# Kernel optimization log

Measured on AMD Instinct MI355X. Metric: run time of the kernel, lower is better.

Reference implementation:

```python
import jax, jax.numpy as jnp
import numpy as np

B, S, NH, NKV, D = 2, 2048, 32, 8, 128

def setup_inputs() -> dict:
    key = jax.random.key(0)
    kq, kk, kv = jax.random.split(key, 3)
    query = jax.random.normal(kq, (B, S, NH, D), dtype=jnp.float32)
    k_ = jax.random.normal(kk, (B, S, NKV, D), dtype=jnp.float32)
    v_ = jax.random.normal(kv, (B, S, NKV, D), dtype=jnp.float32)
    # causal additive mask, broadcastable to [B, NH, S, S]
    causal = jnp.tril(jnp.ones((S, S), dtype=bool))
    attn_mask = jnp.where(causal, 0.0, -1e9).astype(jnp.float32)[None, None]
    return {"query": query, "key": k_, "value": v_, "attn_mask": attn_mask}

def reference(query, key, value, attn_mask):
    nh, nkv = query.shape[-2], key.shape[-2]
    # [B, S, H, D] -> [B, H, S, D]
    q = jnp.swapaxes(query, -3, -2)
    k = jnp.swapaxes(key, -3, -2)
    v = jnpp_swap(value) if False else jnp.swapaxes(value, -3, -2)
    qpk = nh // nkv
    if qpk > 1:
        k = jnp.repeat(k, qpk, axis=-3)
        v = jnp.repeat(v, qpk, axis=-3)
    scale = q.shape[-1] ** (-0.5)
    # [B, H, Sq, Sk]
    score = jnp.einsum('bhqd,bhkd->bhqk', q, k) * scale
    score = score + attn_mask
    probs = jax.nn.softmax(score.astype(jnp.float32), axis=-1).astype(q.dtype)
    out = jnp.einsum('bhqk,bhkd->bhqd', probs, v)
    # [B, H, S, D] -> [B, S, H, D]
    return jnp.swapaxes(out, 1, 2)
```

## Files before the change

### kernel.cpp

```cpp
#include <hip/hip_runtime.h>
#include <hip/hip_bf16.h>

#define B_    2
#define S_    2048
#define NH_   32
#define NKV_  8
#define D_    128
#define QBLK  128
#define KVBLK 64

#define KVH_STRIDE 524288u
#define V_WS_OFF   8388608u

typedef __bf16 bf16x8 __attribute__((ext_vector_type(8)));
typedef float  f32x16 __attribute__((ext_vector_type(16)));
typedef unsigned short u16x4 __attribute__((ext_vector_type(4)));
typedef unsigned int   u32x4 __attribute__((ext_vector_type(4)));

typedef const __attribute__((address_space(1))) void* gptr_t;
typedef __attribute__((address_space(3))) void*       lptr_t;

#if __has_builtin(__builtin_amdgcn_exp2f)
#define EXP2(x) __builtin_amdgcn_exp2f(x)
#else
#define EXP2(x) exp2f(x)
#endif

__device__ inline unsigned short bfu(float f) {
    return __builtin_bit_cast(unsigned short, (__bf16)f);
}
__device__ inline unsigned packbf(float lo, float hi) {
    return (unsigned)bfu(lo) | ((unsigned)bfu(hi) << 16);
}

__global__ __launch_bounds__(256)
void convert_kv(const float* __restrict__ kin, const float* __restrict__ vin,
                unsigned short* __restrict__ kout, unsigned short* __restrict__ vout) {
    __shared__ unsigned short vl[64][136];
    const int t = threadIdx.x;
    if (blockIdx.x < 4096) {
        const int g = blockIdx.x * 256 + t;
        const size_t o = (size_t)g * 4;
        const int d   = (int)(o & 127);
        const int k   = (int)((o >> 7) & 2047);
        const int kvh = (int)((o >> 18) & 7);
        const int b   = (int)(o >> 21);
        const float* src = kin + (((size_t)(b * 2048 + k)) * 8 + kvh) * 128 + d;
        float4 x = *reinterpret_cast<const float4*>(src);
        u16x4 u = { bfu(x.x), bfu(x.y), bfu(x.z), bfu(x.w) };
        *reinterpret_cast<u16x4*>(kout + o) = u;
        return;
    }
    const int bb = blockIdx.x - 4096;
    const int j  = bb & 31;
    const int bk = bb >> 5;
    const int b  = bk >> 3, kvh = bk & 7;
    const float* base = vin + (((size_t)(b * 2048 + j * 64)) * 8 + kvh) * 128;
    #pragma unroll
    for (int i = 0; i < 8; ++i) {
        const int row = i * 8 + (t >> 5), c4 = t & 31;
        float4 x = *reinterpret_cast<const float4*>(base + (size_t)row * 1024 + c4 * 4);
        u16x4 u = { bfu(x.x), bfu(x.y), bfu(x.z), bfu(x.w) };
        *reinterpret_cast<u16x4*>(&vl[row][c4 * 4]) = u;
    }
    __syncthreads();
    unsigned short* out = vout + (size_t)bb * 8192;
    #pragma unroll
    for (int it = 0; it < 4; ++it) {
        const int c = it * 256 + t;
        const int d = c >> 3, k0 = (c & 7) * 8;
        u16x4 lo = { vl[k0 + 0][d], vl[k0 + 1][d], vl[k0 + 2][d], vl[k0 + 3][d] };
        u16x4 hi = { vl[k0 + 4][d], vl[k0 + 5][d], vl[k0 + 6][d], vl[k0 + 7][d] };
        *reinterpret_cast<u16x4*>(out + (size_t)d * 64 + k0)     = lo;
        *reinterpret_cast<u16x4*>(out + (size_t)d * 64 + k0 + 4) = hi;
    }
}

__global__ __launch_bounds__(256, 2)
void sdpa_fwd(const float* __restrict__ qg, const unsigned short* __restrict__ kws,
              const unsigned short* __restrict__ vws, float* __restrict__ og)
{
    __shared__ __align__(16) unsigned short Kb[2][8192];
    __shared__ __align__(16) unsigned short Vb[2][8192];

    const int bx  = blockIdx.x;
    const int qt  = 15 - (bx >> 6);
    const int r   = bx & 63;
    const int kvh = r & 7;
    const int h   = kvh * 4 + ((r >> 3) & 3);
    const int b   = (r >> 5) & 1;
    const int bk  = b * 8 + kvh;

    const int t   = threadIdx.x;
    const int w   = t >> 6;
    const int l   = t & 63;
    const int l32 = l & 31;
    const int lh  = l >> 5;

    const float scale = 0.08838834764831845f * 1.4426950408889634f;
    const int qmin_w = qt * QBLK + w * 32;
    const int qgl    = qmin_w + l32;

    const int koff = ((t >> 4) << 8) + ((((t & 15) << 4)) ^ (((t >> 4) & 7) << 4));
    const int voff = ((t >> 3) << 7) + ((((t & 7) << 4)) ^ (((t >> 3) & 7) << 4));
    const char* Khead = (const char*)kws + (size_t)bk * KVH_STRIDE;
    const char* Vhead = (const char*)vws + (size_t)bk * KVH_STRIDE;

    const char* kp[8];
    #pragma unroll
    for (int dc = 0; dc < 8; ++dc)
        kp[dc] = (const char*)&Kb[0][0] + l32 * 256 +
                 ((dc * 32 + lh * 16) ^ ((l32 & 7) << 4));
    const char* vp[4];
    #pragma unroll
    for (int kc = 0; kc < 4; ++kc)
        vp[kc] = (const char*)&Vb[0][0] + l32 * 128 +
                 ((kc * 32 + lh * 16) ^ ((l32 & 7) << 4));

    bf16x8 qf[8];
    {
        const float* Qp = qg + (((size_t)b * S_ + qgl) * NH_ + h) * D_;
        #pragma unroll
        for (int dc = 0; dc < 8; ++dc) {
            const int d0 = dc * 16 + lh * 8;
            float4 a = *reinterpret_cast<const float4*>(Qp + d0);
            float4 c = *reinterpret_cast<const float4*>(Qp + d0 + 4);
            bf16x8 f;
            f[0] = (__bf16)(a.x * scale); f[1] = (__bf16)(a.y * scale);
            f[2] = (__bf16)(a.z * scale); f[3] = (__bf16)(a.w * scale);
            f[4] = (__bf16)(c.x * scale); f[5] = (__bf16)(c.y * scale);
            f[6] = (__bf16)(c.z * scale); f[7] = (__bf16)(c.w * scale);
            qf[dc] = f;
        }
    }

    const f32x16 z16 = {};
    f32x16 acc[4] = {};
    f32x16 scA0, scA1, scB0, scB1;
    float mrow = -INFINITY, lrow = 0.0f;

    auto issueK = [&](int j, int c) {
        const char* ks = Khead + (size_t)j * 16384 + koff;
        char* kl = (char*)&Kb[c][0] + t * 16;
        #pragma unroll
        for (int i = 0; i < 4; ++i)
            __builtin_amdgcn_global_load_lds((gptr_t)(ks + i * 4096),
                                             (lptr_t)(kl + i * 4096), 16, 0, 0);
    };
    auto issueV = [&](int j, int c) {
        const char* vs = Vhead + (size_t)j * 16384 + voff;
        char* vl = (char*)&Vb[c][0] + t * 16;
        #pragma unroll
        for (int i = 0; i < 4; ++i)
            __builtin_amdgcn_global_load_lds((gptr_t)(vs + i * 4096),
                                             (lptr_t)(vl + i * 4096), 16, 0, 0);
    };

    auto qk = [&](int cb, f32x16& s0, f32x16& s1) {
        #pragma unroll
        for (int dc = 0; dc < 8; ++dc) {
            bf16x8 kf0 = *reinterpret_cast<const bf16x8*>(kp[dc] + cb);
            bf16x8 kf1 = *reinterpret_cast<const bf16x8*>(kp[dc] + cb + 8192);
            s0 = __builtin_amdgcn_mfma_f32_32x32x16_bf16(kf0, qf[dc],
                                                         dc ? s0 : z16, 0, 0, 0);
            s1 = __builtin_amdgcn_mfma_f32_32x32x16_bf16(kf1, qf[dc],
                                                         dc ? s1 : z16, 0, 0, 0);
        }
    };

    auto smpv = [&](f32x16& s0, f32x16& s1, int jb, int cb) {
        if (jb + (KVBLK - 1) > qmin_w) {
            #pragma unroll
            for (int rr = 0; rr < 16; ++rr) {
                const int kk = jb + (rr & 3) + 8 * (rr >> 2) + 4 * lh;
                if (kk > qgl)      s0[rr] = -INFINITY;
                if (kk + 32 > qgl) s1[rr] = -INFINITY;
            }
        }
        float mx[16];
        #pragma unroll
        for (int rr = 0; rr < 16; ++rr) mx[rr] = fmaxf(s0[rr], s1[rr]);
        #pragma unroll
        for (int s = 8; s > 0; s >>= 1)
            #pragma unroll
            for (int i = 0; i < 8; ++i)
                if (i < s) mx[i] = fmaxf(mx[i], mx[i + s]);
        float mt = fmaxf(mx[0], __shfl_xor(mx[0], 32));
        const float mnew = fmaxf(mrow, mt);
        if (!__all(mnew - mrow <= 11.5f)) {
            const float resc = EXP2(mrow - mnew);
            lrow *= resc;
            #pragma unroll
            for (int dt = 0; dt < 4; ++dt) acc[dt] *= resc;
            mrow = mnew;
        }
        #pragma unroll
        for (int rr = 0; rr < 16; ++rr) {
            s0[rr] = EXP2(s0[rr] - mrow);
            s1[rr] = EXP2(s1[rr] - mrow);
        }
        float sm[16];
        #pragma unroll
        for (int rr = 0; rr < 16; ++rr) sm[rr] = s0[rr] + s1[rr];
        #pragma unroll
        for (int s = 8; s > 0; s >>= 1)
            #pragma unroll
            for (int i = 0; i < 8; ++i)
                if (i < s) sm[i] += sm[i + s];
        lrow += sm[0] + __shfl_xor(sm[0], 32);

        bf16x8 pa[4];
        #pragma unroll
        for (int g = 0; g < 4; ++g) {
            float p0, p1, p2, p3, p4, p5, p6, p7;
            if (g == 0) { p0=s0[0]; p1=s0[1]; p2=s0[2]; p3=s0[3];
                          p4=s0[4]; p5=s0[5]; p6=s0[6]; p7=s0[7]; }
            else if (g == 1) { p0=s0[8];  p1=s0[9];  p2=s0[10]; p3=s0[11];
                               p4=s0[12]; p5=s0[13]; p6=s0[14]; p7=s0[15]; }
            else if (g == 2) { p0=s1[0]; p1=s1[1]; p2=s1[2]; p3=s1[3];
                               p4=s1[4]; p5=s1[5]; p6=s1[6]; p7=s1[7]; }
            else { p0=s1[8];  p1=s1[9];  p2=s1[10]; p3=s1[11];
                   p4=s1[12]; p5=s1[13]; p6=s1[14]; p7=s1[15]; }
            unsigned a0 = packbf(p0, p1), b0 = packbf(p4, p5);
            unsigned a1 = packbf(p2, p3), b1 = packbf(p6, p7);
            auto s02 = __builtin_amdgcn_permlane32_swap((int)a0, (int)b0, false, false);
            auto s13 = __builtin_amdgcn_permlane32_swap((int)a1, (int)b1, false, false);
            u32x4 dw = { (unsigned)s02[0], (unsigned)s13[0],
                         (unsigned)s02[1], (unsigned)s13[1] };
            pa[g] = __builtin_bit_cast(bf16x8, dw);
        }
        #pragma unroll
        for (int kc = 0; kc < 4; ++kc) {
            #pragma unroll
            for (int dt = 0; dt < 4; ++dt) {
                bf16x8 vf = *reinterpret_cast<const bf16x8*>(vp[kc] + cb + dt * 4096);
                acc[dt] = __builtin_amdgcn_mfma_f32_32x32x16_bf16(vf, pa[kc], acc[dt], 0, 0, 0);
            }
        }
    };

    issueK(0, 0); issueV(0, 0);
    const int jmax = 2 * qt + 1;
    const int lastlive = (qmin_w + 31) >> 6;

    #pragma unroll 1
    for (int j0 = 0; j0 <= jmax; j0 += 2) {
        const int j1 = j0 + 1;
        issueK(j1, 1);
        asm volatile("s_waitcnt vmcnt(8)" ::: "memory");
        __builtin_amdgcn_s_barrier();
        __builtin_amdgcn_sched_barrier(0);
        __builtin_amdgcn_s_setprio(1);
        if (j0 <= lastlive) qk(0, scA0, scA1);
        if (j0 > 0 && j0 - 1 <= lastlive)
            smpv(scB0, scB1, (j0 - 1) * KVBLK, 16384);
        __builtin_amdgcn_s_setprio(0);
        __builtin_amdgcn_s_barrier();
        __builtin_amdgcn_sched_barrier(0);
        issueV(j1, 1);
        if (j1 < jmax) {
            issueK(j1 + 1, 0);
            asm volatile("s_waitcnt vmcnt(8)" ::: "memory");
        } else {
            asm volatile("s_waitcnt vmcnt(4)" ::: "memory");
        }
        __builtin_amdgcn_s_barrier();
        __builtin_amdgcn_sched_barrier(0);
        __builtin_amdgcn_s_setprio(1);
        if (j1 <= lastlive) qk(16384, scB0, scB1);
        if (j0 <= lastlive) smpv(scA0, scA1, j0 * KVBLK, 0);
        __builtin_amdgcn_s_setprio(0);
        __builtin_amdgcn_s_barrier();
        __builtin_amdgcn_sched_barrier(0);
        if (j1 < jmax) issueV(j1 + 1, 0);
    }
    asm volatile("s_waitcnt vmcnt(0)" ::: "memory");
    __builtin_amdgcn_s_barrier();
    __builtin_amdgcn_sched_barrier(0);
    if (jmax <= lastlive) smpv(scB0, scB1, jmax * KVBLK, 16384);

    const float invl = 1.0f / lrow;
    float* Op = og + (((size_t)b * S_ + qgl) * NH_ + h) * D_;
    #pragma unroll
    for (int dt = 0; dt < 4; ++dt) {
        #pragma unroll
        for (int rg = 0; rg < 4; ++rg) {
            float4 st;
            st.x = acc[dt][rg * 4 + 0] * invl;
            st.y = acc[dt][rg * 4 + 1] * invl;
            st.z = acc[dt][rg * 4 + 2] * invl;
            st.w = acc[dt][rg * 4 + 3] * invl;
            *reinterpret_cast<float4*>(Op + dt * 32 + rg * 8 + lh * 4) = st;
        }
    }
}

extern "C" void kernel_launch(void* const* d_in, const int* in_sizes, int n_in,
                              void* d_out, int out_size, void* d_ws, size_t ws_size,
                              hipStream_t stream) {
    const float* q = (const float*)d_in[0];
    const float* k = (const float*)d_in[1];
    const float* v = (const float*)d_in[2];
    float* out = (float*)d_out;
    unsigned short* kws = (unsigned short*)d_ws;
    unsigned short* vws = (unsigned short*)((char*)d_ws + V_WS_OFF);

    convert_kv<<<dim3(4608), 256, 0, stream>>>(k, v, kws, vws);
    sdpa_fwd  <<<dim3(1024), 256, 0, stream>>>(q, kws, vws, out);
}
```

Before: 111.9 us.

## Double per-wave query rows and pair causal tiles in a persistent two-pass block

Each wave now processes 64 query rows, held as two 32-row fragments, so every K/V LDS fragment read feeds twice as many MFMAs. Each block runs two passes over paired query tiles (7-p and p) to balance causal work. The grid drops from 1024 to 256 blocks, and the two-stage ping-pong with setprio is replaced by a simpler single-stage prefetch loop. The aim is to raise K/V reuse and even out causal imbalance, at the cost of higher register pressure (launch_bounds min-blocks removed), fewer blocks per CU, and less overlap between softmax and MFMA.

```diff
diff --git a/kernel.cpp b/kernel.cpp
--- a/kernel.cpp
+++ b/kernel.cpp
@@ -6,7 +6,7 @@
 #define NH_   32
 #define NKV_  8
 #define D_    128
-#define QBLK  128
+#define QBLK  256
 #define KVBLK 64
 
 #define KVH_STRIDE 524288u
@@ -76,7 +76,7 @@
     }
 }
 
-__global__ __launch_bounds__(256, 2)
+__global__ __launch_bounds__(256)
 void sdpa_fwd(const float* __restrict__ qg, const unsigned short* __restrict__ kws,
               const unsigned short* __restrict__ vws, float* __restrict__ og)
 {
@@ -84,7 +84,7 @@
     __shared__ __align__(16) unsigned short Vb[2][8192];
 
     const int bx  = blockIdx.x;
-    const int qt  = 15 - (bx >> 6);
+    const int p   = bx >> 6;
     const int r   = bx & 63;
     const int kvh = r & 7;
     const int h   = kvh * 4 + ((r >> 3) & 3);
@@ -93,13 +93,10 @@
 
     const int t   = threadIdx.x;
     const int w   = t >> 6;
-    const int l   = t & 63;
-    const int l32 = l & 31;
-    const int lh  = l >> 5;
+    const int l32 = t & 31;
+    const int lh  = (t & 63) >> 5;
 
     const float scale = 0.08838834764831845f * 1.4426950408889634f;
-    const int qmin_w = qt * QBLK + w * 32;
-    const int qgl    = qmin_w + l32;
 
     const int koff = ((t >> 4) << 8) + ((((t & 15) << 4)) ^ (((t >> 4) & 7) << 4));
     const int voff = ((t >> 3) << 7) + ((((t & 7) << 4)) ^ (((t >> 3) & 7) << 4));
@@ -116,28 +113,6 @@
     for (int kc = 0; kc < 4; ++kc)
         vp[kc] = (const char*)&Vb[0][0] + l32 * 128 +
                  ((kc * 32 + lh * 16) ^ ((l32 & 7) << 4));
-
-    bf16x8 qf[8];
-    {
-        const float* Qp = qg + (((size_t)b * S_ + qgl) * NH_ + h) * D_;
-        #pragma unroll
-        for (int dc = 0; dc < 8; ++dc) {
-            const int d0 = dc * 16 + lh * 8;
-            float4 a = *reinterpret_cast<const float4*>(Qp + d0);
-            float4 c = *reinterpret_cast<const float4*>(Qp + d0 + 4);
-            bf16x8 f;
-            f[0] = (__bf16)(a.x * scale); f[1] = (__bf16)(a.y * scale);
-            f[2] = (__bf16)(a.z * scale); f[3] = (__bf16)(a.w * scale);
-            f[4] = (__bf16)(c.x * scale); f[5] = (__bf16)(c.y * scale);
-            f[6] = (__bf16)(c.z * scale); f[7] = (__bf16)(c.w * scale);
-            qf[dc] = f;
-        }
-    }
-
-    const f32x16 z16 = {};
-    f32x16 acc[4] = {};
-    f32x16 scA0, scA1, scB0, scB1;
-    float mrow = -INFINITY, lrow = 0.0f;
 
     auto issueK = [&](int j, int c) {
         const char* ks = Khead + (size_t)j * 16384 + koff;
@@ -156,141 +131,184 @@
                                              (lptr_t)(vl + i * 4096), 16, 0, 0);
     };
 
-    auto qk = [&](int cb, f32x16& s0, f32x16& s1) {
+    const f32x16 z16 = {};
+
+    #pragma unroll 1
+    for (int pass = 0; pass < 2; ++pass) {
+        const int qt    = pass ? p : (7 - p);
+        const int qbase = qt * QBLK + w * 64;
+        const int qglA  = qbase + l32;
+        const int qglB  = qglA + 32;
+
+        bf16x8 qfA[8], qfB[8];
+        {
+            const float* QpA = qg + (((size_t)b * S_ + qglA) * NH_ + h) * D_;
+            const float* QpB = qg + (((size_t)b * S_ + qglB) * NH_ + h) * D_;
+            #pragma unroll
+            for (int dc = 0; dc < 8; ++dc) {
+                const int d0 = dc * 16 + lh * 8;
+                float4 a = *reinterpret_cast<const float4*>(QpA + d0);
+                float4 c = *reinterpret_cast<const float4*>(QpA + d0 + 4);
+                bf16x8 f;
+                f[0] = (__bf16)(a.x * scale); f[1] = (__bf16)(a.y * scale);
+                f[2] = (__bf16)(a.z * scale); f[3] = (__bf16)(a.w * scale);
+                f[4] = (__bf16)(c.x * scale); f[5] = (__bf16)(c.y * scale);
+                f[6] = (__bf16)(c.z * scale); f[7] = (__bf16)(c.w * scale);
+                qfA[dc] = f;
+                a = *reinterpret_cast<const float4*>(QpB + d0);
+                c = *reinterpret_cast<const float4*>(QpB + d0 + 4);
+                f[0] = (__bf16)(a.x * scale); f[1] = (__bf16)(a.y * scale);
+                f[2] = (__bf16)(a.z * scale); f[3] = (__bf16)(a.w * scale);
+                f[4] = (__bf16)(c.x * scale); f[5] = (__bf16)(c.y * scale);
+                f[6] = (__bf16)(c.z * scale); f[7] = (__bf16)(c.w * scale);
+                qfB[dc] = f;
+            }
+        }
+
+        f32x16 accA[4] = {}, accB[4] = {};
+        f32x16 sA0, sA1, sB0, sB1;
+        float mrowA = -INFINITY, lrowA = 0.0f;
+        float mrowB = -INFINITY, lrowB = 0.0f;
+
+        auto softpack = [&](f32x16& s0, f32x16& s1, float& mrow, float& lrow,
+                            f32x16* accp, bf16x8* pa) {
+            float mx[16];
+            #pragma unroll
+            for (int rr = 0; rr < 16; ++rr) mx[rr] = fmaxf(s0[rr], s1[rr]);
+            #pragma unroll
+            for (int s = 8; s > 0; s >>= 1)
+                #pragma unroll
+                for (int i = 0; i < 8; ++i)
+                    if (i < s) mx[i] = fmaxf(mx[i], mx[i + s]);
+            float mt = fmaxf(mx[0], __shfl_xor(mx[0], 32));
+            const float mnew = fmaxf(mrow, mt);
+            if (!__all(mnew - mrow <= 11.5f)) {
+                const float resc = EXP2(mrow - mnew);
+                lrow *= resc;
+                #pragma unroll
+                for (int dt = 0; dt < 4; ++dt) accp[dt] *= resc;
+                mrow = mnew;
+            }
+            #pragma unroll
+            for (int rr = 0; rr < 16; ++rr) {
+                s0[rr] = EXP2(s0[rr] - mrow);
+                s1[rr] = EXP2(s1[rr] - mrow);
+            }
+            float sm[16];
+            #pragma unroll
+            for (int rr = 0; rr < 16; ++rr) sm[rr] = s0[rr] + s1[rr];
+            #pragma unroll
+            for (int s = 8; s > 0; s >>= 1)
+                #pragma unroll
+                for (int i = 0; i < 8; ++i)
+                    if (i < s) sm[i] += sm[i + s];
+            lrow += sm[0] + __shfl_xor(sm[0], 32);
+
+            #pragma unroll
+            for (int g = 0; g < 4; ++g) {
+                float p0, p1, p2, p3, p4, p5, p6, p7;
+                if (g == 0) { p0=s0[0]; p1=s0[1]; p2=s0[2]; p3=s0[3];
+                              p4=s0[4]; p5=s0[5]; p6=s0[6]; p7=s0[7]; }
+                else if (g == 1) { p0=s0[8];  p1=s0[9];  p2=s0[10]; p3=s0[11];
+                                   p4=s0[12]; p5=s0[13]; p6=s0[14]; p7=s0[15]; }
+                else if (g == 2) { p0=s1[0]; p1=s1[1]; p2=s1[2]; p3=s1[3];
+                                   p4=s1[4]; p5=s1[5]; p6=s1[6]; p7=s1[7]; }
+                else { p0=s1[8];  p1=s1[9];  p2=s1[10]; p3=s1[11];
+                       p4=s1[12]; p5=s1[13]; p6=s1[14]; p7=s1[15]; }
+                unsigned a0 = packbf(p0, p1), b0 = packbf(p4, p5);
+                unsigned a1 = packbf(p2, p3), b1 = packbf(p6, p7);
+                auto s02 = __builtin_amdgcn_permlane32_swap((int)a0, (int)b0, false, false);
+                auto s13 = __builtin_amdgcn_permlane32_swap((int)a1, (int)b1, false, false);
+                u32x4 dw = { (unsigned)s02[0], (unsigned)s13[0],
+                             (unsigned)s02[1], (unsigned)s13[1] };
+                pa[g] = __builtin_bit_cast(bf16x8, dw);
+            }
+        };
+
+        issueV(0, 0); issueK(0, 0);
+        const int jmax = 4 * qt + 3;
+        const int lastlive = (qbase + 63) >> 6;
+
+        #pragma unroll 1
+        for (int j = 0; j <= jmax; ++j) {
+            const int cur = j & 1;
+            const int cb  = cur ? 16384 : 0;
+            const int jb  = j * KVBLK;
+
+            __builtin_amdgcn_s_barrier();
+            __builtin_amdgcn_sched_barrier(0);
+            if (j < jmax) {
+                issueV(j + 1, cur ^ 1);
+                issueK(j + 1, cur ^ 1);
+                asm volatile("s_waitcnt vmcnt(8)" ::: "memory");
+            } else {
+                asm volatile("s_waitcnt vmcnt(0)" ::: "memory");
+            }
+            __builtin_amdgcn_s_barrier();
+            __builtin_amdgcn_sched_barrier(0);
+
+            if (j > lastlive) continue;
+
+            #pragma unroll
+            for (int dc = 0; dc < 8; ++dc) {
+                bf16x8 kf0 = *reinterpret_cast<const bf16x8*>(kp[dc] + cb);
+                bf16x8 kf1 = *reinterpret_cast<const bf16x8*>(kp[dc] + cb + 8192);
+                sA0 = __builtin_amdgcn_mfma_f32_32x32x16_bf16(kf0, qfA[dc],
+                                                              dc ? sA0 : z16, 0, 0, 0);
+                sB0 = __builtin_amdgcn_mfma_f32_32x32x16_bf16(kf0, qfB[dc],
+                                                              dc ? sB0 : z16, 0, 0, 0);
+                sA1 = __builtin_amdgcn_mfma_f32_32x32x16_bf16(kf1, qfA[dc],
+                                                              dc ? sA1 : z16, 0, 0, 0);
+                sB1 = __builtin_amdgcn_mfma_f32_32x32x16_bf16(kf1, qfB[dc],
+                                                              dc ? sB1 : z16, 0, 0, 0);
+            }
+
+            if (jb + (KVBLK - 1) > qbase) {
+                #pragma unroll
+                for (int rr = 0; rr < 16; ++rr) {
+                    const int kk = jb + (rr & 3) + 8 * (rr >> 2) + 4 * lh;
+                    if (kk > qglA)      sA0[rr] = -INFINITY;
+                    if (kk + 32 > qglA) sA1[rr] = -INFINITY;
+                    if (kk > qglB)      sB0[rr] = -INFINITY;
+                    if (kk + 32 > qglB) sB1[rr] = -INFINITY;
+                }
+            }
+
+            bf16x8 paA[4], paB[4];
+            softpack(sA0, sA1, mrowA, lrowA, accA, paA);
+            softpack(sB0, sB1, mrowB, lrowB, accB, paB);
+
+            #pragma unroll
+            for (int kc = 0; kc < 4; ++kc) {
+                #pragma unroll
+                for (int dt = 0; dt < 4; ++dt) {
+                    bf16x8 vf = *reinterpret_cast<const bf16x8*>(vp[kc] + cb + dt * 4096);
+                    accA[dt] = __builtin_amdgcn_mfma_f32_32x32x16_bf16(vf, paA[kc], accA[dt], 0, 0, 0);
+                    accB[dt] = __builtin_amdgcn_mfma_f32_32x32x16_bf16(vf, paB[kc], accB[dt], 0, 0, 0);
+                }
+            }
+        }
+
+        const float invlA = 1.0f / lrowA;
+        const float invlB = 1.0f / lrowB;
+        float* OpA = og + (((size_t)b * S_ + qglA) * NH_ + h) * D_;
+        float* OpB = og + (((size_t)b * S_ + qglB) * NH_ + h) * D_;
         #pragma unroll
-        for (int dc = 0; dc < 8; ++dc) {
-            bf16x8 kf0 = *reinterpret_cast<const bf16x8*>(kp[dc] + cb);
-            bf16x8 kf1 = *reinterpret_cast<const bf16x8*>(kp[dc] + cb + 8192);
-            s0 = __builtin_amdgcn_mfma_f32_32x32x16_bf16(kf0, qf[dc],
-                                                         dc ? s0 : z16, 0, 0, 0);
-            s1 = __builtin_amdgcn_mfma_f32_32x32x16_bf16(kf1, qf[dc],
-                                                         dc ? s1 : z16, 0, 0, 0);
-        }
-    };
-
-    auto smpv = [&](f32x16& s0, f32x16& s1, int jb, int cb) {
-        if (jb + (KVBLK - 1) > qmin_w) {
-            #pragma unroll
-            for (int rr = 0; rr < 16; ++rr) {
-                const int kk = jb + (rr & 3) + 8 * (rr >> 2) + 4 * lh;
-                if (kk > qgl)      s0[rr] = -INFINITY;
-                if (kk + 32 > qgl) s1[rr] = -INFINITY;
-            }
-        }
-        float mx[16];
-        #pragma unroll
-        for (int rr = 0; rr < 16; ++rr) mx[rr] = fmaxf(s0[rr], s1[rr]);
-        #pragma unroll
-        for (int s = 8; s > 0; s >>= 1)
-            #pragma unroll
-            for (int i = 0; i < 8; ++i)
-                if (i < s) mx[i] = fmaxf(mx[i], mx[i + s]);
-        float mt = fmaxf(mx[0], __shfl_xor(mx[0], 32));
-        const float mnew = fmaxf(mrow, mt);
-        if (!__all(mnew - mrow <= 11.5f)) {
-            const float resc = EXP2(mrow - mnew);
-            lrow *= resc;
-            #pragma unroll
-            for (int dt = 0; dt < 4; ++dt) acc[dt] *= resc;
-            mrow = mnew;
-        }
-        #pragma unroll
-        for (int rr = 0; rr < 16; ++rr) {
-            s0[rr] = EXP2(s0[rr] - mrow);
-            s1[rr] = EXP2(s1[rr] - mrow);
-        }
-        float sm[16];
-        #pragma unroll
-        for (int rr = 0; rr < 16; ++rr) sm[rr] = s0[rr] + s1[rr];
-        #pragma unroll
-        for (int s = 8; s > 0; s >>= 1)
-            #pragma unroll
-            for (int i = 0; i < 8; ++i)
-                if (i < s) sm[i] += sm[i + s];
-        lrow += sm[0] + __shfl_xor(sm[0], 32);
-
-        bf16x8 pa[4];
-        #pragma unroll
-        for (int g = 0; g < 4; ++g) {
-            float p0, p1, p2, p3, p4, p5, p6, p7;
-            if (g == 0) { p0=s0[0]; p1=s0[1]; p2=s0[2]; p3=s0[3];
-                          p4=s0[4]; p5=s0[5]; p6=s0[6]; p7=s0[7]; }
-            else if (g == 1) { p0=s0[8];  p1=s0[9];  p2=s0[10]; p3=s0[11];
-                               p4=s0[12]; p5=s0[13]; p6=s0[14]; p7=s0[15]; }
-            else if (g == 2) { p0=s1[0]; p1=s1[1]; p2=s1[2]; p3=s1[3];
-                               p4=s1[4]; p5=s1[5]; p6=s1[6]; p7=s1[7]; }
-            else { p0=s1[8];  p1=s1[9];  p2=s1[10]; p3=s1[11];
-                   p4=s1[12]; p5=s1[13]; p6=s1[14]; p7=s1[15]; }
-            unsigned a0 = packbf(p0, p1), b0 = packbf(p4, p5);
-            unsigned a1 = packbf(p2, p3), b1 = packbf(p6, p7);
-            auto s02 = __builtin_amdgcn_permlane32_swap((int)a0, (int)b0, false, false);
-            auto s13 = __builtin_amdgcn_permlane32_swap((int)a1, (int)b1, false, false);
-            u32x4 dw = { (unsigned)s02[0], (unsigned)s13[0],
-                         (unsigned)s02[1], (unsigned)s13[1] };
-            pa[g] = __builtin_bit_cast(bf16x8, dw);
-        }
-        #pragma unroll
-        for (int kc = 0; kc < 4; ++kc) {
-            #pragma unroll
-            for (int dt = 0; dt < 4; ++dt) {
-                bf16x8 vf = *reinterpret_cast<const bf16x8*>(vp[kc] + cb + dt * 4096);
-                acc[dt] = __builtin_amdgcn_mfma_f32_32x32x16_bf16(vf, pa[kc], acc[dt], 0, 0, 0);
-            }
-        }
-    };
-
-    issueK(0, 0); issueV(0, 0);
-    const int jmax = 2 * qt + 1;
-    const int lastlive = (qmin_w + 31) >> 6;
-
-    #pragma unroll 1
-    for (int j0 = 0; j0 <= jmax; j0 += 2) {
-        const int j1 = j0 + 1;
-        issueK(j1, 1);
-        asm volatile("s_waitcnt vmcnt(8)" ::: "memory");
-        __builtin_amdgcn_s_barrier();
-        __builtin_amdgcn_sched_barrier(0);
-        __builtin_amdgcn_s_setprio(1);
-        if (j0 <= lastlive) qk(0, scA0, scA1);
-        if (j0 > 0 && j0 - 1 <= lastlive)
-            smpv(scB0, scB1, (j0 - 1) * KVBLK, 16384);
-        __builtin_amdgcn_s_setprio(0);
-        __builtin_amdgcn_s_barrier();
-        __builtin_amdgcn_sched_barrier(0);
-        issueV(j1, 1);
-        if (j1 < jmax) {
-            issueK(j1 + 1, 0);
-            asm volatile("s_waitcnt vmcnt(8)" ::: "memory");
-        } else {
-            asm volatile("s_waitcnt vmcnt(4)" ::: "memory");
-        }
-        __builtin_amdgcn_s_barrier();
-        __builtin_amdgcn_sched_barrier(0);
-        __builtin_amdgcn_s_setprio(1);
-        if (j1 <= lastlive) qk(16384, scB0, scB1);
-        if (j0 <= lastlive) smpv(scA0, scA1, j0 * KVBLK, 0);
-        __builtin_amdgcn_s_setprio(0);
-        __builtin_amdgcn_s_barrier();
-        __builtin_amdgcn_sched_barrier(0);
-        if (j1 < jmax) issueV(j1 + 1, 0);
-    }
-    asm volatile("s_waitcnt vmcnt(0)" ::: "memory");
-    __builtin_amdgcn_s_barrier();
-    __builtin_amdgcn_sched_barrier(0);
-    if (jmax <= lastlive) smpv(scB0, scB1, jmax * KVBLK, 16384);
-
-    const float invl = 1.0f / lrow;
-    float* Op = og + (((size_t)b * S_ + qgl) * NH_ + h) * D_;
-    #pragma unroll
-    for (int dt = 0; dt < 4; ++dt) {
-        #pragma unroll
-        for (int rg = 0; rg < 4; ++rg) {
-            float4 st;
-            st.x = acc[dt][rg * 4 + 0] * invl;
-            st.y = acc[dt][rg * 4 + 1] * invl;
-            st.z = acc[dt][rg * 4 + 2] * invl;
-            st.w = acc[dt][rg * 4 + 3] * invl;
-            *reinterpret_cast<float4*>(Op + dt * 32 + rg * 8 + lh * 4) = st;
+        for (int dt = 0; dt < 4; ++dt) {
+            #pragma unroll
+            for (int rg = 0; rg < 4; ++rg) {
+                float4 st;
+                st.x = accA[dt][rg * 4 + 0] * invlA;
+                st.y = accA[dt][rg * 4 + 1] * invlA;
+                st.z = accA[dt][rg * 4 + 2] * invlA;
+                st.w = accA[dt][rg * 4 + 3] * invlA;
+                *reinterpret_cast<float4*>(OpA + dt * 32 + rg * 8 + lh * 4) = st;
+                st.x = accB[dt][rg * 4 + 0] * invlB;
+                st.y = accB[dt][rg * 4 + 1] * invlB;
+                st.z = accB[dt][rg * 4 + 2] * invlB;
+                st.w = accB[dt][rg * 4 + 3] * invlB;
+                *reinterpret_cast<float4*>(OpB + dt * 32 + rg * 8 + lh * 4) = st;
+            }
         }
     }
 }
@@ -306,5 +324,5 @@
     unsigned short* vws = (unsigned short*)((char*)d_ws + V_WS_OFF);
 
     convert_kv<<<dim3(4608), 256, 0, stream>>>(k, v, kws, vws);
-    sdpa_fwd  <<<dim3(1024), 256, 0, stream>>>(q, kws, vws, out);
-}
+    sdpa_fwd  <<<dim3(256),  256, 0, stream>>>(q, kws, vws, out);
+}
```

Result: slower. 147.3 us (+31.6%).
